# Kernel optimization log

Measured on AMD Instinct MI355X. Metric: run time of the kernel, lower is better.

The kernel has to match this reference:

```python
import jax, jax.numpy as jnp
import numpy as np

B, N, DIM, H, DH = 2, 2048, 1024, 16, 64
INNER = H * DH
ROPE_BASE = 10000.0


def setup_inputs() -> dict:
    key = jax.random.key(0)
    ks = jax.random.split(key, 6)
    s = 0.02
    return {
        "x": jax.random.normal(ks[0], (B, N, DIM), jnp.float32),
        "Wq": jax.random.normal(ks[1], (DIM, INNER), jnp.float32) * s,
        "Wk": jax.random.normal(ks[2], (DIM, INNER), jnp.float32) * s,
        "Wv": jax.random.normal(ks[3], (DIM, INNER), jnp.float32) * s,
        "Wo": jax.random.normal(ks[4], (INNER, DIM), jnp.float32) * s,
        "bo": jnp.zeros((DIM,), jnp.float32),
    }


def _rotate_half(x):
    # einops '... (d r) -> ... d r' with r=2: x1 = even lanes, x2 = odd lanes,
    # then cat((-x2, x1), dim=-1)
    x1 = x[..., 0::2]
    x2 = x[..., 1::2]
    return jnp.concatenate([-x2, x1], axis=-1)


def _rope_sin_cos(n, d, dtype):
    # inv_freq over arange(0, d, 2); emb = cat(f, f) -> length d
    inv_freq = 1.0 / (ROPE_BASE ** (jnp.arange(0, d, 2, dtype=jnp.float32) / d))
    f = jnp.arange(n, dtype=jnp.float32)[:, None] * inv_freq[None, :]  # [n, d/2]
    e = jnp.concatenate([f, f], axis=-1)  # [n, d]
    return jnp.sin(e).astype(dtype), jnp.cos(e).astype(dtype)


def _apply_rope(t, sin, cos):
    # t: [b, h, n, d]; sin/cos: [n, d]; rot_dim == d (full head), t_pass empty
    return t * cos[None, None] + _rotate_half(t) * sin[None, None]


def reference(x, Wq, Wk, Wv, Wo, bo):
    b, n, _ = x.shape
    scale = DH ** (-0.5)

    def split_heads(y):  # [b, n, h*d] -> [b, h, n, d]
        return y.reshape(b, n, H, DH).transpose(0, 2, 1, 3)

    q = split_heads(x @ Wq)
    k = split_heads(x @ Wk)
    v = split_heads(x @ Wv)

    sin, cos = _rope_sin_cos(n, DH, x.dtype)
    q = _apply_rope(q, sin, cos)
    k = _apply_rope(k, sin, cos)

    # causal SDPA (mask=None path -> is_causal=True), eval mode so dropout_p=0
    scores = jnp.einsum("bhqd,bhkd->bhqk", q, k) * scale
    causal = jnp.tril(jnp.ones((n, n), dtype=bool))
    scores = jnp.where(causal[None, None], scores, jnp.finfo(scores.dtype).min)
    probs = jax.nn.softmax(scores, axis=-1)
    attn = jnp.einsum("bhqk,bhkd->bhqd", probs, v)

    out = attn.transpose(0, 2, 1, 3).reshape(b, n, INNER) @ Wo + bo
    return out, k, v
```

## Files before the change

kernel.cpp:

```cpp
#include <hip/hip_runtime.h>
#include <cstdint>
#include <cmath>

#define BB   2
#define NN   2048
#define DIMM 1024
#define NHH  16
#define DHH  64
#define MMR  (BB * NN)

typedef _Float16 half8  __attribute__((ext_vector_type(8)));
typedef _Float16 half4v __attribute__((ext_vector_type(4)));
typedef float    f32x4  __attribute__((ext_vector_type(4)));

#define GLD16(gp, lp)                                                          \
  __builtin_amdgcn_global_load_lds(                                            \
      (const __attribute__((address_space(1))) unsigned int*)(gp),             \
      (__attribute__((address_space(3))) unsigned int*)(lp), 16, 0, 0)

__global__ __launch_bounds__(256) void cvt_x_kernel(const float* __restrict__ x,
                                                    _Float16* __restrict__ xh) {
  int i = (blockIdx.x * 256 + threadIdx.x) * 4;
  float4 v = *(const float4*)(x + i);
  half4v h;
  h[0] = (_Float16)v.x; h[1] = (_Float16)v.y;
  h[2] = (_Float16)v.z; h[3] = (_Float16)v.w;
  *(half4v*)(xh + i) = h;
}

__global__ __launch_bounds__(256) void transpose_w_kernel(
    const float* __restrict__ Wq, const float* __restrict__ Wk,
    const float* __restrict__ Wv, const float* __restrict__ Wo,
    _Float16* __restrict__ wt) {
  __shared__ float tile[64][65];
  int z = blockIdx.z;
  const float* W = (z == 0) ? Wq : (z == 1) ? Wk : (z == 2) ? Wv : Wo;
  _Float16* dst = wt + (size_t)z * 1024 * 1024;
  int r0 = blockIdx.x * 64;
  int c0 = blockIdx.y * 64;
  int t = threadIdx.x;
  int tr = t >> 4;
  int tc = (t & 15) * 4;
#pragma unroll
  for (int i = 0; i < 4; ++i) {
    float4 v = *(const float4*)(W + (size_t)(r0 + tr + i * 16) * 1024 + c0 + tc);
    tile[tr + i * 16][tc + 0] = v.x;
    tile[tr + i * 16][tc + 1] = v.y;
    tile[tr + i * 16][tc + 2] = v.z;
    tile[tr + i * 16][tc + 3] = v.w;
  }
  __syncthreads();
#pragma unroll
  for (int i = 0; i < 4; ++i) {
    int nl = tr + i * 16;
    half4v hv;
    hv[0] = (_Float16)tile[tc + 0][nl];
    hv[1] = (_Float16)tile[tc + 1][nl];
    hv[2] = (_Float16)tile[tc + 2][nl];
    hv[3] = (_Float16)tile[tc + 3][nl];
    *(half4v*)(dst + (size_t)(c0 + nl) * 1024 + r0 + tc) = hv;
  }
}

__global__ __launch_bounds__(256) void gemm_qkv_kernel(
    const _Float16* __restrict__ xh, const _Float16* __restrict__ wt,
    float* __restrict__ ko, float* __restrict__ vo,
    _Float16* __restrict__ qh, _Float16* __restrict__ kh,
    _Float16* __restrict__ vth) {
  __shared__ __align__(16) char smem[32768];
  _Float16* As = (_Float16*)smem;
  _Float16* Bs = (_Float16*)(smem + 16384);
  float (*Cs)[65] = (float(*)[65])smem;

  const int m0  = blockIdx.x * 64;
  const int ngl = blockIdx.y * 64;
  const int mat = ngl >> 10;
  const int n0  = ngl & 1023;
  const _Float16* wb = wt + (size_t)mat * 1024 * 1024;
  const int t = threadIdx.x;
  const int wv = t >> 6, lane = t & 63, l16 = lane & 15, quad = lane >> 4;
  const int r  = t >> 3;
  const int cl = t & 7;
  const int csw = (cl ^ (r & 7)) * 8;
  const _Float16* pa0 = xh + (size_t)(m0 + r) * 1024 + csw;
  const _Float16* pa1 = pa0 + 32 * 1024;
  const _Float16* pb0 = wb + (size_t)(n0 + r) * 1024 + csw;
  const _Float16* pb1 = pb0 + 32 * 1024;
  f32x4 acc[4] = {};
  const int arow = wv * 16 + l16;
  const int a7 = arow & 7;
  GLD16(pa0, As + wv * 512);
  GLD16(pa1, As + 2048 + wv * 512);
  GLD16(pb0, Bs + wv * 512);
  GLD16(pb1, Bs + 2048 + wv * 512);
  int cur = 0;
  for (int k0 = 0; k0 < 1024; k0 += 64) {
    if (k0 + 64 < 1024) {
      const int nb = cur ^ 1;
      GLD16(pa0 + k0 + 64, As + nb * 4096 + wv * 512);
      GLD16(pa1 + k0 + 64, As + nb * 4096 + 2048 + wv * 512);
      GLD16(pb0 + k0 + 64, Bs + nb * 4096 + wv * 512);
      GLD16(pb1 + k0 + 64, Bs + nb * 4096 + 2048 + wv * 512);
      asm volatile("s_waitcnt vmcnt(4)" ::: "memory");
    } else {
      asm volatile("s_waitcnt vmcnt(0)" ::: "memory");
    }
    __builtin_amdgcn_s_barrier();
    asm volatile("" ::: "memory");
    const _Float16* Ab = As + cur * 4096;
    const _Float16* Bb = Bs + cur * 4096;
    half8 af0 = *(const half8*)(Ab + arow * 64 + (quad ^ a7) * 8);
    half8 af1 = *(const half8*)(Ab + arow * 64 + ((4 + quad) ^ a7) * 8);
#pragma unroll
    for (int nt = 0; nt < 4; ++nt) {
      int brow = nt * 16 + l16;
      int b7 = brow & 7;
      half8 bf0 = *(const half8*)(Bb + brow * 64 + (quad ^ b7) * 8);
      half8 bf1 = *(const half8*)(Bb + brow * 64 + ((4 + quad) ^ b7) * 8);
      acc[nt] = __builtin_amdgcn_mfma_f32_16x16x32_f16(af0, bf0, acc[nt], 0, 0, 0);
      acc[nt] = __builtin_amdgcn_mfma_f32_16x16x32_f16(af1, bf1, acc[nt], 0, 0, 0);
    }
    asm volatile("s_waitcnt lgkmcnt(0)" ::: "memory");
    __builtin_amdgcn_s_barrier();
    asm volatile("" ::: "memory");
    cur ^= 1;
  }
#pragma unroll
  for (int nt = 0; nt < 4; ++nt)
#pragma unroll
    for (int rr = 0; rr < 4; ++rr)
      Cs[wv * 16 + quad * 4 + rr][nt * 16 + l16] = acc[nt][rr];
  __syncthreads();
  int lr = t >> 2;
  int cseg = (t & 3) * 16;
  int m = m0 + lr;
  int b = m >> 11;
  int pos = m & 2047;
  int h = n0 >> 6;
  int bhh = b * NHH + h;
  float vals[16];
  if (mat == 2) {
#pragma unroll
    for (int j = 0; j < 16; ++j) vals[j] = Cs[lr][cseg + j];
  } else {
    float fpos = (float)pos;
#pragma unroll
    for (int j = 0; j < 16; ++j) {
      int i = cseg + j;
      int jd = (i < 32) ? i : (i - 32);
      float invf = exp2f((float)jd * -0.41524101186092029f);
      float ang = fpos * invf;
      float sv, cv;
      sincosf(ang, &sv, &cv);
      float partner = (i < 32) ? -Cs[lr][2 * i + 1] : Cs[lr][2 * (i - 32)];
      vals[j] = Cs[lr][i] * cv + partner * sv;
    }
  }
  size_t rowb = ((size_t)bhh * NN + pos) * DHH + cseg;
  if (mat == 0) {
    half8 h0, h1;
#pragma unroll
    for (int j = 0; j < 8; ++j) { h0[j] = (_Float16)(vals[j] * 0.125f); h1[j] = (_Float16)(vals[8 + j] * 0.125f); }
    *(half8*)(qh + rowb) = h0;
    *(half8*)(qh + rowb + 8) = h1;
  } else if (mat == 1) {
#pragma unroll
    for (int j4 = 0; j4 < 4; ++j4) {
      float4 o;
      o.x = vals[j4 * 4 + 0]; o.y = vals[j4 * 4 + 1];
      o.z = vals[j4 * 4 + 2]; o.w = vals[j4 * 4 + 3];
      *(float4*)(ko + rowb + j4 * 4) = o;
    }
    half8 h0, h1;
#pragma unroll
    for (int j = 0; j < 8; ++j) { h0[j] = (_Float16)vals[j]; h1[j] = (_Float16)vals[8 + j]; }
    *(half8*)(kh + rowb) = h0;
    *(half8*)(kh + rowb + 8) = h1;
  } else {
#pragma unroll
    for (int j4 = 0; j4 < 4; ++j4) {
      float4 o;
      o.x = vals[j4 * 4 + 0]; o.y = vals[j4 * 4 + 1];
      o.z = vals[j4 * 4 + 2]; o.w = vals[j4 * 4 + 3];
      *(float4*)(vo + rowb + j4 * 4) = o;
    }
#pragma unroll
    for (int j = 0; j < 16; ++j)
      vth[((size_t)bhh * DHH + cseg + j) * NN + pos] = (_Float16)vals[j];
  }
}

__global__ __launch_bounds__(256, 2) void fattn_kernel(
    const _Float16* __restrict__ qh, const _Float16* __restrict__ kh,
    const _Float16* __restrict__ vth, _Float16* __restrict__ ah) {
  __shared__ __align__(16) _Float16 Kt[3][4096];
  __shared__ __align__(16) _Float16 Vt[3][4096];
  __shared__ __align__(16) _Float16 Pb[4][16][72];
  const int lin  = (int)blockIdx.x;
  const int xcd  = lin & 7;
  const int slot = lin >> 3;
  const int bh   = xcd * 4 + (slot & 3);
  const int pair = slot >> 2;
  const int t = threadIdx.x;
  const int wv = t >> 6, lane = t & 63, l16 = lane & 15, quad = lane >> 4;
  const int b = bh >> 4, h = bh & 15;
  const _Float16* kg = kh + (size_t)bh * NN * DHH;
  const _Float16* vg = vth + (size_t)bh * DHH * NN;
  half8 ones;
#pragma unroll
  for (int j = 0; j < 8; ++j) ones[j] = (_Float16)1.f;

#define STAGE_KV(tile, nb) do {                                                \
    const _Float16* kn_ = kg + (size_t)(tile) * 64 * DHH;                      \
    const _Float16* vn_ = vg + (tile) * 64;                                    \
    _Float16* kl_ = &Kt[nb][0];                                                \
    _Float16* vl_ = &Vt[nb][0];                                                \
    _Pragma("unroll")                                                          \
    for (int iss = 0; iss < 2; ++iss) {                                        \
      int cid = iss * 256 + wv * 64 + lane;                                    \
      int row = cid >> 3;                                                      \
      int c = (cid & 7) ^ (row & 7);                                           \
      GLD16(kn_ + (size_t)row * DHH + c * 8, kl_ + (iss * 256 + wv * 64) * 8); \
      GLD16(vn_ + (size_t)row * NN + c * 8, vl_ + (iss * 256 + wv * 64) * 8);  \
    }                                                                          \
  } while (0)

  for (int job = 0; job < 2; ++job) {
    const int qb = (job == 0) ? (15 - pair) : pair;
    const int q0 = qb * 128;
    half8 qf[2][2];
#pragma unroll
    for (int qt2 = 0; qt2 < 2; ++qt2) {
      const _Float16* qp =
          qh + ((size_t)bh * NN + q0 + wv * 32 + qt2 * 16 + l16) * DHH + quad * 8;
      qf[qt2][0] = *(const half8*)qp;
      qf[qt2][1] = *(const half8*)(qp + 32);
    }
    f32x4 o[2][4] = {};
    f32x4 ls[2] = {};
    const int ktmax = 2 * qb + 1;
    STAGE_KV(0, 0);
    STAGE_KV(1, 1);
    int cur = 0;
    for (int kt = 0; kt <= ktmax; ++kt) {
      if (kt + 2 <= ktmax) {
        int nb = cur + 2; if (nb >= 3) nb -= 3;
        STAGE_KV(kt + 2, nb);
        asm volatile("s_waitcnt vmcnt(8)" ::: "memory");
      } else if (kt + 1 <= ktmax) {
        asm volatile("s_waitcnt vmcnt(4)" ::: "memory");
      } else {
        asm volatile("s_waitcnt vmcnt(0)" ::: "memory");
      }
      __builtin_amdgcn_s_barrier();
      asm volatile("" ::: "memory");
      if (kt * 64 <= q0 + wv * 32 + 31) {
        half8 kf[4][2], vf[4][2];
        const _Float16* Kb = &Kt[cur][0];
        const _Float16* Vb = &Vt[cur][0];
#pragma unroll
        for (int nt = 0; nt < 4; ++nt) {
          int row = nt * 16 + l16;
          int r7 = row & 7;
          kf[nt][0] = *(const half8*)(Kb + row * 64 + ((quad ^ r7) * 8));
          kf[nt][1] = *(const half8*)(Kb + row * 64 + (((quad + 4) ^ r7) * 8));
          vf[nt][0] = *(const half8*)(Vb + row * 64 + ((quad ^ r7) * 8));
          vf[nt][1] = *(const half8*)(Vb + row * 64 + (((quad + 4) ^ r7) * 8));
        }
#pragma unroll
        for (int qt2 = 0; qt2 < 2; ++qt2) {
          int base = q0 + wv * 32 + qt2 * 16;
          if (kt * 64 <= base + 15) {
            f32x4 s4[4];
#pragma unroll
            for (int nt = 0; nt < 4; ++nt) {
              f32x4 z = {};
              z = __builtin_amdgcn_mfma_f32_16x16x32_f16(qf[qt2][0], kf[nt][0], z, 0, 0, 0);
              s4[nt] = __builtin_amdgcn_mfma_f32_16x16x32_f16(qf[qt2][1], kf[nt][1], z, 0, 0, 0);
            }
            if (kt * 64 + 63 > base) {
#pragma unroll
              for (int nt = 0; nt < 4; ++nt) {
                int key = kt * 64 + nt * 16 + l16;
#pragma unroll
                for (int r = 0; r < 4; ++r) {
                  float p = (key > base + quad * 4 + r) ? 0.f : __expf(s4[nt][r]);
                  Pb[wv][quad * 4 + r][nt * 16 + l16] = (_Float16)p;
                }
              }
            } else {
#pragma unroll
              for (int nt = 0; nt < 4; ++nt)
#pragma unroll
                for (int r = 0; r < 4; ++r)
                  Pb[wv][quad * 4 + r][nt * 16 + l16] = (_Float16)__expf(s4[nt][r]);
            }
            asm volatile("s_waitcnt lgkmcnt(0)" ::: "memory");
            half8 pf0 = *(const half8*)&Pb[wv][l16][quad * 8];
            half8 pf1 = *(const half8*)&Pb[wv][l16][32 + quad * 8];
#pragma unroll
            for (int nt = 0; nt < 4; ++nt) {
              o[qt2][nt] = __builtin_amdgcn_mfma_f32_16x16x32_f16(pf0, vf[nt][0], o[qt2][nt], 0, 0, 0);
              o[qt2][nt] = __builtin_amdgcn_mfma_f32_16x16x32_f16(pf1, vf[nt][1], o[qt2][nt], 0, 0, 0);
            }
            ls[qt2] = __builtin_amdgcn_mfma_f32_16x16x32_f16(pf0, ones, ls[qt2], 0, 0, 0);
            ls[qt2] = __builtin_amdgcn_mfma_f32_16x16x32_f16(pf1, ones, ls[qt2], 0, 0, 0);
          }
        }
      }
      asm volatile("s_waitcnt lgkmcnt(0)" ::: "memory");
      __builtin_amdgcn_s_barrier();
      asm volatile("" ::: "memory");
      cur = (cur == 2) ? 0 : cur + 1;
    }
#pragma unroll
    for (int qt2 = 0; qt2 < 2; ++qt2)
#pragma unroll
      for (int r = 0; r < 4; ++r) {
        float inv = 1.f / ls[qt2][r];
        int pos = q0 + wv * 32 + qt2 * 16 + quad * 4 + r;
        size_t ob = ((size_t)(b * NN + pos)) * DIMM + h * DHH;
#pragma unroll
        for (int nt = 0; nt < 4; ++nt)
          ah[ob + nt * 16 + l16] = (_Float16)(o[qt2][nt][r] * inv);
      }
  }
#undef STAGE_KV
}

__global__ __launch_bounds__(256) void gemm_out_kernel(
    const _Float16* __restrict__ ah, const _Float16* __restrict__ wot,
    const float* __restrict__ bo, float* __restrict__ out) {
  __shared__ __align__(16) char smem[32768];
  _Float16* As = (_Float16*)smem;
  _Float16* Bs = (_Float16*)(smem + 16384);
  const int m0 = blockIdx.x * 64;
  const int n0 = blockIdx.y * 64;
  const int t = threadIdx.x;
  const int wv = t >> 6, lane = t & 63, l16 = lane & 15, quad = lane >> 4;
  const int r  = t >> 3;
  const int cl = t & 7;
  const int csw = (cl ^ (r & 7)) * 8;
  const _Float16* pa0 = ah + (size_t)(m0 + r) * 1024 + csw;
  const _Float16* pa1 = pa0 + 32 * 1024;
  const _Float16* pb0 = wot + (size_t)(n0 + r) * 1024 + csw;
  const _Float16* pb1 = pb0 + 32 * 1024;
  f32x4 acc[4] = {};
  const int arow = wv * 16 + l16;
  const int a7 = arow & 7;
  GLD16(pa0, As + wv * 512);
  GLD16(pa1, As + 2048 + wv * 512);
  GLD16(pb0, Bs + wv * 512);
  GLD16(pb1, Bs + 2048 + wv * 512);
  int cur = 0;
  for (int k0 = 0; k0 < 1024; k0 += 64) {
    if (k0 + 64 < 1024) {
      const int nb = cur ^ 1;
      GLD16(pa0 + k0 + 64, As + nb * 4096 + wv * 512);
      GLD16(pa1 + k0 + 64, As + nb * 4096 + 2048 + wv * 512);
      GLD16(pb0 + k0 + 64, Bs + nb * 4096 + wv * 512);
      GLD16(pb1 + k0 + 64, Bs + nb * 4096 + 2048 + wv * 512);
      asm volatile("s_waitcnt vmcnt(4)" ::: "memory");
    } else {
      asm volatile("s_waitcnt vmcnt(0)" ::: "memory");
    }
    __builtin_amdgcn_s_barrier();
    asm volatile("" ::: "memory");
    const _Float16* Ab = As + cur * 4096;
    const _Float16* Bb = Bs + cur * 4096;
    half8 af0 = *(const half8*)(Ab + arow * 64 + (quad ^ a7) * 8);
    half8 af1 = *(const half8*)(Ab + arow * 64 + ((4 + quad) ^ a7) * 8);
#pragma unroll
    for (int nt = 0; nt < 4; ++nt) {
      int brow = nt * 16 + l16;
      int b7 = brow & 7;
      half8 bf0 = *(const half8*)(Bb + brow * 64 + (quad ^ b7) * 8);
      half8 bf1 = *(const half8*)(Bb + brow * 64 + ((4 + quad) ^ b7) * 8);
      acc[nt] = __builtin_amdgcn_mfma_f32_16x16x32_f16(af0, bf0, acc[nt], 0, 0, 0);
      acc[nt] = __builtin_amdgcn_mfma_f32_16x16x32_f16(af1, bf1, acc[nt], 0, 0, 0);
    }
    asm volatile("s_waitcnt lgkmcnt(0)" ::: "memory");
    __builtin_amdgcn_s_barrier();
    asm volatile("" ::: "memory");
    cur ^= 1;
  }
#pragma unroll
  for (int nt = 0; nt < 4; ++nt) {
    int col = n0 + nt * 16 + l16;
    float bias = bo[col];
#pragma unroll
    for (int rr = 0; rr < 4; ++rr) {
      out[(size_t)(m0 + wv * 16 + quad * 4 + rr) * 1024 + col] = acc[nt][rr] + bias;
    }
  }
}

extern "C" void kernel_launch(void* const* d_in, const int* in_sizes, int n_in,
                              void* d_out, int out_size, void* d_ws, size_t ws_size,
                              hipStream_t stream) {
  (void)in_sizes; (void)n_in; (void)out_size; (void)ws_size;
  const float* x  = (const float*)d_in[0];
  const float* Wq = (const float*)d_in[1];
  const float* Wk = (const float*)d_in[2];
  const float* Wv = (const float*)d_in[3];
  const float* Wo = (const float*)d_in[4];
  const float* bo = (const float*)d_in[5];

  float* out = (float*)d_out;
  float* ko  = out + (size_t)MMR * DIMM;
  float* vo  = ko + (size_t)BB * NHH * NN * DHH;

  char* w = (char*)d_ws;
  _Float16* xh  = (_Float16*)w;
  _Float16* ah  = (_Float16*)w;
  _Float16* wt  = (_Float16*)(w + (8u << 20));
  _Float16* qh  = (_Float16*)(w + (16u << 20));
  _Float16* kh  = (_Float16*)(w + (24u << 20));
  _Float16* vth = (_Float16*)(w + (32u << 20));

  hipLaunchKernelGGL(cvt_x_kernel, dim3(4096), dim3(256), 0, stream, x, xh);
  hipLaunchKernelGGL(transpose_w_kernel, dim3(16, 16, 4), dim3(256), 0, stream,
                     Wq, Wk, Wv, Wo, wt);
  hipLaunchKernelGGL(gemm_qkv_kernel, dim3(64, 48), dim3(256), 0, stream,
                     xh, wt, ko, vo, qh, kh, vth);
  hipLaunchKernelGGL(fattn_kernel, dim3(256), dim3(256), 0, stream,
                     qh, kh, vth, ah);
  hipLaunchKernelGGL(gemm_out_kernel, dim3(64, 16), dim3(256), 0, stream,
                     ah, wt + (size_t)3 * 1024 * 1024, bo, out);
}
```

Before: 207.4 us.

## Triple-buffer GEMM K-loop and use 8 waves of 16 query rows in attention

Both GEMM kernels move from double to triple-buffered LDS staging, with loads issued two k-steps ahead and vmcnt waits adjusted, to hide more global-load latency. The flash-attention kernel now launches 512 threads: each of 8 waves owns 16 query rows instead of 32, and each thread issues one K/V staging load per tile instead of two. This is meant to raise parallelism per block and cut per-wave register pressure. In exchange, GEMM LDS use grows to 48KB, which can reduce occupancy, and attention K/V fragments are now read from LDS by twice as many waves.

```diff
diff --git a/kernel.cpp b/kernel.cpp
--- a/kernel.cpp
+++ b/kernel.cpp
@@ -67,9 +67,9 @@
     float* __restrict__ ko, float* __restrict__ vo,
     _Float16* __restrict__ qh, _Float16* __restrict__ kh,
     _Float16* __restrict__ vth) {
-  __shared__ __align__(16) char smem[32768];
+  __shared__ __align__(16) char smem[49152];
   _Float16* As = (_Float16*)smem;
-  _Float16* Bs = (_Float16*)(smem + 16384);
+  _Float16* Bs = (_Float16*)(smem + 24576);
   float (*Cs)[65] = (float(*)[65])smem;
 
   const int m0  = blockIdx.x * 64;
@@ -89,18 +89,23 @@
   f32x4 acc[4] = {};
   const int arow = wv * 16 + l16;
   const int a7 = arow & 7;
-  GLD16(pa0, As + wv * 512);
-  GLD16(pa1, As + 2048 + wv * 512);
-  GLD16(pb0, Bs + wv * 512);
-  GLD16(pb1, Bs + 2048 + wv * 512);
+
+#define STAGE_AB(k0s, nb) do {                                                 \
+    GLD16(pa0 + (k0s), As + (nb) * 4096 + wv * 512);                           \
+    GLD16(pa1 + (k0s), As + (nb) * 4096 + 2048 + wv * 512);                    \
+    GLD16(pb0 + (k0s), Bs + (nb) * 4096 + wv * 512);                           \
+    GLD16(pb1 + (k0s), Bs + (nb) * 4096 + 2048 + wv * 512);                    \
+  } while (0)
+
+  STAGE_AB(0, 0);
+  STAGE_AB(64, 1);
   int cur = 0;
   for (int k0 = 0; k0 < 1024; k0 += 64) {
-    if (k0 + 64 < 1024) {
-      const int nb = cur ^ 1;
-      GLD16(pa0 + k0 + 64, As + nb * 4096 + wv * 512);
-      GLD16(pa1 + k0 + 64, As + nb * 4096 + 2048 + wv * 512);
-      GLD16(pb0 + k0 + 64, Bs + nb * 4096 + wv * 512);
-      GLD16(pb1 + k0 + 64, Bs + nb * 4096 + 2048 + wv * 512);
+    if (k0 + 128 < 1024) {
+      int nb = cur + 2; if (nb >= 3) nb -= 3;
+      STAGE_AB(k0 + 128, nb);
+      asm volatile("s_waitcnt vmcnt(8)" ::: "memory");
+    } else if (k0 + 64 < 1024) {
       asm volatile("s_waitcnt vmcnt(4)" ::: "memory");
     } else {
       asm volatile("s_waitcnt vmcnt(0)" ::: "memory");
@@ -123,8 +128,9 @@
     asm volatile("s_waitcnt lgkmcnt(0)" ::: "memory");
     __builtin_amdgcn_s_barrier();
     asm volatile("" ::: "memory");
-    cur ^= 1;
-  }
+    cur = (cur == 2) ? 0 : cur + 1;
+  }
+#undef STAGE_AB
 #pragma unroll
   for (int nt = 0; nt < 4; ++nt)
 #pragma unroll
@@ -190,12 +196,12 @@
   }
 }
 
-__global__ __launch_bounds__(256, 2) void fattn_kernel(
+__global__ __launch_bounds__(512) void fattn_kernel(
     const _Float16* __restrict__ qh, const _Float16* __restrict__ kh,
     const _Float16* __restrict__ vth, _Float16* __restrict__ ah) {
   __shared__ __align__(16) _Float16 Kt[3][4096];
   __shared__ __align__(16) _Float16 Vt[3][4096];
-  __shared__ __align__(16) _Float16 Pb[4][16][72];
+  __shared__ __align__(16) _Float16 Pb[8][16][72];
   const int lin  = (int)blockIdx.x;
   const int xcd  = lin & 7;
   const int slot = lin >> 3;
@@ -206,6 +212,8 @@
   const int b = bh >> 4, h = bh & 15;
   const _Float16* kg = kh + (size_t)bh * NN * DHH;
   const _Float16* vg = vth + (size_t)bh * DHH * NN;
+  const int srow = t >> 3;
+  const int sc   = ((t & 7) ^ (srow & 7)) * 8;
   half8 ones;
 #pragma unroll
   for (int j = 0; j < 8; ++j) ones[j] = (_Float16)1.f;
@@ -213,31 +221,23 @@
 #define STAGE_KV(tile, nb) do {                                                \
     const _Float16* kn_ = kg + (size_t)(tile) * 64 * DHH;                      \
     const _Float16* vn_ = vg + (tile) * 64;                                    \
-    _Float16* kl_ = &Kt[nb][0];                                                \
-    _Float16* vl_ = &Vt[nb][0];                                                \
-    _Pragma("unroll")                                                          \
-    for (int iss = 0; iss < 2; ++iss) {                                        \
-      int cid = iss * 256 + wv * 64 + lane;                                    \
-      int row = cid >> 3;                                                      \
-      int c = (cid & 7) ^ (row & 7);                                           \
-      GLD16(kn_ + (size_t)row * DHH + c * 8, kl_ + (iss * 256 + wv * 64) * 8); \
-      GLD16(vn_ + (size_t)row * NN + c * 8, vl_ + (iss * 256 + wv * 64) * 8);  \
-    }                                                                          \
+    GLD16(kn_ + (size_t)srow * DHH + sc, &Kt[nb][0] + (wv * 64) * 8);          \
+    GLD16(vn_ + (size_t)srow * NN + sc, &Vt[nb][0] + (wv * 64) * 8);           \
   } while (0)
 
   for (int job = 0; job < 2; ++job) {
     const int qb = (job == 0) ? (15 - pair) : pair;
     const int q0 = qb * 128;
-    half8 qf[2][2];
-#pragma unroll
-    for (int qt2 = 0; qt2 < 2; ++qt2) {
+    const int base = q0 + wv * 16;
+    half8 qf0, qf1;
+    {
       const _Float16* qp =
-          qh + ((size_t)bh * NN + q0 + wv * 32 + qt2 * 16 + l16) * DHH + quad * 8;
-      qf[qt2][0] = *(const half8*)qp;
-      qf[qt2][1] = *(const half8*)(qp + 32);
-    }
-    f32x4 o[2][4] = {};
-    f32x4 ls[2] = {};
+          qh + ((size_t)bh * NN + base + l16) * DHH + quad * 8;
+      qf0 = *(const half8*)qp;
+      qf1 = *(const half8*)(qp + 32);
+    }
+    f32x4 o[4] = {};
+    f32x4 ls = {};
     const int ktmax = 2 * qb + 1;
     STAGE_KV(0, 0);
     STAGE_KV(1, 1);
@@ -246,15 +246,15 @@
       if (kt + 2 <= ktmax) {
         int nb = cur + 2; if (nb >= 3) nb -= 3;
         STAGE_KV(kt + 2, nb);
-        asm volatile("s_waitcnt vmcnt(8)" ::: "memory");
+        asm volatile("s_waitcnt vmcnt(4)" ::: "memory");
       } else if (kt + 1 <= ktmax) {
-        asm volatile("s_waitcnt vmcnt(4)" ::: "memory");
+        asm volatile("s_waitcnt vmcnt(2)" ::: "memory");
       } else {
         asm volatile("s_waitcnt vmcnt(0)" ::: "memory");
       }
       __builtin_amdgcn_s_barrier();
       asm volatile("" ::: "memory");
-      if (kt * 64 <= q0 + wv * 32 + 31) {
+      if (kt * 64 <= base + 15) {
         half8 kf[4][2], vf[4][2];
         const _Float16* Kb = &Kt[cur][0];
         const _Float16* Vb = &Vt[cur][0];
@@ -267,46 +267,40 @@
           vf[nt][0] = *(const half8*)(Vb + row * 64 + ((quad ^ r7) * 8));
           vf[nt][1] = *(const half8*)(Vb + row * 64 + (((quad + 4) ^ r7) * 8));
         }
-#pragma unroll
-        for (int qt2 = 0; qt2 < 2; ++qt2) {
-          int base = q0 + wv * 32 + qt2 * 16;
-          if (kt * 64 <= base + 15) {
-            f32x4 s4[4];
-#pragma unroll
-            for (int nt = 0; nt < 4; ++nt) {
-              f32x4 z = {};
-              z = __builtin_amdgcn_mfma_f32_16x16x32_f16(qf[qt2][0], kf[nt][0], z, 0, 0, 0);
-              s4[nt] = __builtin_amdgcn_mfma_f32_16x16x32_f16(qf[qt2][1], kf[nt][1], z, 0, 0, 0);
+        f32x4 s4[4];
+#pragma unroll
+        for (int nt = 0; nt < 4; ++nt) {
+          f32x4 z = {};
+          z = __builtin_amdgcn_mfma_f32_16x16x32_f16(qf0, kf[nt][0], z, 0, 0, 0);
+          s4[nt] = __builtin_amdgcn_mfma_f32_16x16x32_f16(qf1, kf[nt][1], z, 0, 0, 0);
+        }
+        if (kt * 64 + 63 > base) {
+#pragma unroll
+          for (int nt = 0; nt < 4; ++nt) {
+            int key = kt * 64 + nt * 16 + l16;
+#pragma unroll
+            for (int r = 0; r < 4; ++r) {
+              float p = (key > base + quad * 4 + r) ? 0.f : __expf(s4[nt][r]);
+              Pb[wv][quad * 4 + r][nt * 16 + l16] = (_Float16)p;
             }
-            if (kt * 64 + 63 > base) {
-#pragma unroll
-              for (int nt = 0; nt < 4; ++nt) {
-                int key = kt * 64 + nt * 16 + l16;
-#pragma unroll
-                for (int r = 0; r < 4; ++r) {
-                  float p = (key > base + quad * 4 + r) ? 0.f : __expf(s4[nt][r]);
-                  Pb[wv][quad * 4 + r][nt * 16 + l16] = (_Float16)p;
-                }
-              }
-            } else {
-#pragma unroll
-              for (int nt = 0; nt < 4; ++nt)
-#pragma unroll
-                for (int r = 0; r < 4; ++r)
-                  Pb[wv][quad * 4 + r][nt * 16 + l16] = (_Float16)__expf(s4[nt][r]);
-            }
-            asm volatile("s_waitcnt lgkmcnt(0)" ::: "memory");
-            half8 pf0 = *(const half8*)&Pb[wv][l16][quad * 8];
-            half8 pf1 = *(const half8*)&Pb[wv][l16][32 + quad * 8];
-#pragma unroll
-            for (int nt = 0; nt < 4; ++nt) {
-              o[qt2][nt] = __builtin_amdgcn_mfma_f32_16x16x32_f16(pf0, vf[nt][0], o[qt2][nt], 0, 0, 0);
-              o[qt2][nt] = __builtin_amdgcn_mfma_f32_16x16x32_f16(pf1, vf[nt][1], o[qt2][nt], 0, 0, 0);
-            }
-            ls[qt2] = __builtin_amdgcn_mfma_f32_16x16x32_f16(pf0, ones, ls[qt2], 0, 0, 0);
-            ls[qt2] = __builtin_amdgcn_mfma_f32_16x16x32_f16(pf1, ones, ls[qt2], 0, 0, 0);
           }
+        } else {
+#pragma unroll
+          for (int nt = 0; nt < 4; ++nt)
+#pragma unroll
+            for (int r = 0; r < 4; ++r)
+              Pb[wv][quad * 4 + r][nt * 16 + l16] = (_Float16)__expf(s4[nt][r]);
         }
+        asm volatile("s_waitcnt lgkmcnt(0)" ::: "memory");
+        half8 pf0 = *(const half8*)&Pb[wv][l16][quad * 8];
+        half8 pf1 = *(const half8*)&Pb[wv][l16][32 + quad * 8];
+#pragma unroll
+        for (int nt = 0; nt < 4; ++nt) {
+          o[nt] = __builtin_amdgcn_mfma_f32_16x16x32_f16(pf0, vf[nt][0], o[nt], 0, 0, 0);
+          o[nt] = __builtin_amdgcn_mfma_f32_16x16x32_f16(pf1, vf[nt][1], o[nt], 0, 0, 0);
+        }
+        ls = __builtin_amdgcn_mfma_f32_16x16x32_f16(pf0, ones, ls, 0, 0, 0);
+        ls = __builtin_amdgcn_mfma_f32_16x16x32_f16(pf1, ones, ls, 0, 0, 0);
       }
       asm volatile("s_waitcnt lgkmcnt(0)" ::: "memory");
       __builtin_amdgcn_s_barrier();
@@ -314,16 +308,14 @@
       cur = (cur == 2) ? 0 : cur + 1;
     }
 #pragma unroll
-    for (int qt2 = 0; qt2 < 2; ++qt2)
-#pragma unroll
-      for (int r = 0; r < 4; ++r) {
-        float inv = 1.f / ls[qt2][r];
-        int pos = q0 + wv * 32 + qt2 * 16 + quad * 4 + r;
-        size_t ob = ((size_t)(b * NN + pos)) * DIMM + h * DHH;
-#pragma unroll
-        for (int nt = 0; nt < 4; ++nt)
-          ah[ob + nt * 16 + l16] = (_Float16)(o[qt2][nt][r] * inv);
-      }
+    for (int r = 0; r < 4; ++r) {
+      float inv = 1.f / ls[r];
+      int pos = base + quad * 4 + r;
+      size_t ob = ((size_t)(b * NN + pos)) * DIMM + h * DHH;
+#pragma unroll
+      for (int nt = 0; nt < 4; ++nt)
+        ah[ob + nt * 16 + l16] = (_Float16)(o[nt][r] * inv);
+    }
   }
 #undef STAGE_KV
 }
@@ -331,9 +323,9 @@
 __global__ __launch_bounds__(256) void gemm_out_kernel(
     const _Float16* __restrict__ ah, const _Float16* __restrict__ wot,
     const float* __restrict__ bo, float* __restrict__ out) {
-  __shared__ __align__(16) char smem[32768];
+  __shared__ __align__(16) char smem[49152];
   _Float16* As = (_Float16*)smem;
-  _Float16* Bs = (_Float16*)(smem + 16384);
+  _Float16* Bs = (_Float16*)(smem + 24576);
   const int m0 = blockIdx.x * 64;
   const int n0 = blockIdx.y * 64;
   const int t = threadIdx.x;
@@ -348,18 +340,23 @@
   f32x4 acc[4] = {};
   const int arow = wv * 16 + l16;
   const int a7 = arow & 7;
-  GLD16(pa0, As + wv * 512);
-  GLD16(pa1, As + 2048 + wv * 512);
-  GLD16(pb0, Bs + wv * 512);
-  GLD16(pb1, Bs + 2048 + wv * 512);
+
+#define STAGE_AB(k0s, nb) do {                                                 \
+    GLD16(pa0 + (k0s), As + (nb) * 4096 + wv * 512);                           \
+    GLD16(pa1 + (k0s), As + (nb) * 4096 + 2048 + wv * 512);                    \
+    GLD16(pb0 + (k0s), Bs + (nb) * 4096 + wv * 512);                           \
+    GLD16(pb1 + (k0s), Bs + (nb) * 4096 + 2048 + wv * 512);                    \
+  } while (0)
+
+  STAGE_AB(0, 0);
+  STAGE_AB(64, 1);
   int cur = 0;
   for (int k0 = 0; k0 < 1024; k0 += 64) {
-    if (k0 + 64 < 1024) {
-      const int nb = cur ^ 1;
-      GLD16(pa0 + k0 + 64, As + nb * 4096 + wv * 512);
-      GLD16(pa1 + k0 + 64, As + nb * 4096 + 2048 + wv * 512);
-      GLD16(pb0 + k0 + 64, Bs + nb * 4096 + wv * 512);
-      GLD16(pb1 + k0 + 64, Bs + nb * 4096 + 2048 + wv * 512);
+    if (k0 + 128 < 1024) {
+      int nb = cur + 2; if (nb >= 3) nb -= 3;
+      STAGE_AB(k0 + 128, nb);
+      asm volatile("s_waitcnt vmcnt(8)" ::: "memory");
+    } else if (k0 + 64 < 1024) {
       asm volatile("s_waitcnt vmcnt(4)" ::: "memory");
     } else {
       asm volatile("s_waitcnt vmcnt(0)" ::: "memory");
@@ -382,8 +379,9 @@
     asm volatile("s_waitcnt lgkmcnt(0)" ::: "memory");
     __builtin_amdgcn_s_barrier();
     asm volatile("" ::: "memory");
-    cur ^= 1;
-  }
+    cur = (cur == 2) ? 0 : cur + 1;
+  }
+#undef STAGE_AB
 #pragma unroll
   for (int nt = 0; nt < 4; ++nt) {
     int col = n0 + nt * 16 + l16;
@@ -423,7 +421,7 @@
                      Wq, Wk, Wv, Wo, wt);
   hipLaunchKernelGGL(gemm_qkv_kernel, dim3(64, 48), dim3(256), 0, stream,
                      xh, wt, ko, vo, qh, kh, vth);
-  hipLaunchKernelGGL(fattn_kernel, dim3(256), dim3(256), 0, stream,
+  hipLaunchKernelGGL(fattn_kernel, dim3(256), dim3(512), 0, stream,
                      qh, kh, vth, ah);
   hipLaunchKernelGGL(gemm_out_kernel, dim3(64, 16), dim3(256), 0, stream,
                      ah, wt + (size_t)3 * 1024 * 1024, bo, out);
```

Measured after the change: 212.4 us. 1.02x slower.
